# Optimization experiments

Measured on AMD Instinct MI355X. Metric: run time of the kernel, lower is better.

## Reference

```python
import jax, jax.numpy as jnp
import numpy as np

H = 1024  # hidden size

def _gru_layer(x, h0_l, w_ih_l, w_hh_l, b_ih_l, b_hh_l):
    # x: [T,B,I]; precompute input gates for all timesteps (like addmm in the kernel)
    x_gates = jnp.einsum('tbi,gi->tbg', x, w_ih_l) + b_ih_l  # [T,B,3H]

    def step(h, xg):
        # h: [B,H]; xg: [B,3H]
        h_gates = h @ w_hh_l.T + b_hh_l  # [B,3H]
        xr, xz, xn = xg[:, :H], xg[:, H:2*H], xg[:, 2*H:]
        hr, hz, hn = h_gates[:, :H], h_gates[:, H:2*H], h_gates[:, 2*H:]
        r = jax.nn.sigmoid(xr + hr)
        z = jax.nn.sigmoid(xz + hz)
        n = jnp.tanh(xn + r * hn)
        h_new = (1.0 - z) * n + z * h
        return h_new, h_new

    h_final, seq_out = jax.lax.scan(step, h0_l, x_gates)
    return h_final, seq_out


def setup_inputs() -> dict:
    key = jax.random.key(0)
    ks = jax.random.split(key, 6)
    T, B, I, L = 512, 64, 1024, 2
    s = 1.0 / np.sqrt(H)
    return {
        'x': jax.random.normal(ks[0], (T, B, I), dtype=jnp.float32),
        'h0': jax.random.normal(ks[1], (L, B, H), dtype=jnp.float32),
        'w_ih': jax.random.normal(ks[2], (L, 3 * H, I), dtype=jnp.float32) * s,
        'w_hh': jax.random.normal(ks[3], (L, 3 * H, H), dtype=jnp.float32) * s,
        'b_ih': jax.random.normal(ks[4], (L, 3 * H), dtype=jnp.float32) * s,
        'b_hh': jax.random.normal(ks[5], (L, 3 * H), dtype=jnp.float32) * s,
    }


def reference(x, h0, w_ih, w_hh, b_ih, b_hh):
    num_layers = h0.shape[0]
    h_n = []
    cur = x
    for l in range(num_layers):
        h_final, seq_out = _gru_layer(cur, h0[l], w_ih[l], w_hh[l], b_ih[l], b_hh[l])
        h_n.append(h_final)
        cur = seq_out  # layer output becomes next layer's input
    # kernel returns only the final hidden state of every layer, in fp32
    return jnp.stack(h_n, axis=0)  # [L,B,H]
```

## Files before the change

### kernel.cpp

```cpp
#include <hip/hip_runtime.h>

typedef unsigned short u16;
typedef unsigned long long u64;
typedef __attribute__((ext_vector_type(8))) short short8;
typedef __attribute__((ext_vector_type(4))) float f32x4;

#define HH 1024
#define BB 64
#define TT 512
#define G3 3072
#define NBLK 192
#define NS 513
#define SLOT (BB * HH)
#define FSTRIDE 32

__device__ __forceinline__ u16 f2b(float f) {
  unsigned u = __float_as_uint(f);
  unsigned r = (u + 0x7fffu + ((u >> 16) & 1u)) >> 16;
  return (u16)r;
}
__device__ __forceinline__ float b2f(u16 h) {
  return __uint_as_float(((unsigned)h) << 16);
}

__device__ __forceinline__ void st_u32_agent(unsigned* p, unsigned v) {
  __hip_atomic_store(p, v, __ATOMIC_RELAXED, __HIP_MEMORY_SCOPE_AGENT);
}
__device__ __forceinline__ unsigned ld_u32_agent(const unsigned* p) {
  return __hip_atomic_load(p, __ATOMIC_RELAXED, __HIP_MEMORY_SCOPE_AGENT);
}


__global__ void f32_to_bf16_k(const float* __restrict__ s, u16* __restrict__ d, int n) {
  int stride = gridDim.x * blockDim.x * 4;
  for (int i = (blockIdx.x * blockDim.x + threadIdx.x) * 4; i < n; i += stride) {
    float4 v = *(const float4*)(s + i);
    uint2 p;
    p.x = (unsigned)f2b(v.x) | ((unsigned)f2b(v.y) << 16);
    p.y = (unsigned)f2b(v.z) | ((unsigned)f2b(v.w) << 16);
    *(uint2*)(d + i) = p;
  }
}

__global__ void init_h_k(const float* __restrict__ h0in, u16* __restrict__ hbuf0,
                         u16* __restrict__ hbuf1) {
  int i = blockIdx.x * blockDim.x + threadIdx.x;
  if (i < BB * HH) {
    hbuf0[i] = f2b(h0in[i]);
    hbuf1[i] = f2b(h0in[BB * HH + i]);
  }
}


__global__ __launch_bounds__(256) void gemm_xg_k(
    const u16* __restrict__ A, const u16* __restrict__ Wt,
    const float* __restrict__ bias, u16* __restrict__ C) {
  const int bm = blockIdx.x / 24;
  const int bn = blockIdx.x % 24;
  const int m0 = bm * 128, n0 = bn * 128;
  __shared__ __align__(16) u16 al[128 * 40];
  __shared__ __align__(16) u16 bl[128 * 40];
  const int tid = threadIdx.x;
  const int w = tid >> 6, l = tid & 63;
  const int wr = w >> 1, wc = w & 1;
  const int c0 = tid, c1 = tid + 256;
  const int r0 = c0 >> 2, s0 = c0 & 3, r1 = c1 >> 2, s1 = c1 & 3;

  const f32x4 fzero = {0.f, 0.f, 0.f, 0.f};
  f32x4 acc[4][4];
#pragma unroll
  for (int i = 0; i < 4; ++i)
#pragma unroll
    for (int j = 0; j < 4; ++j) acc[i][j] = fzero;

  const u16* a0p = A + (size_t)(m0 + r0) * 1024 + s0 * 8;
  const u16* a1p = A + (size_t)(m0 + r1) * 1024 + s1 * 8;
  const u16* b0p = Wt + (size_t)(n0 + r0) * 1024 + s0 * 8;
  const u16* b1p = Wt + (size_t)(n0 + r1) * 1024 + s1 * 8;

  int4 va0 = *(const int4*)(a0p);
  int4 va1 = *(const int4*)(a1p);
  int4 vb0 = *(const int4*)(b0p);
  int4 vb1 = *(const int4*)(b1p);

  for (int kt = 0; kt < 32; ++kt) {
    __syncthreads();
    *(int4*)&al[r0 * 40 + s0 * 8] = va0;
    *(int4*)&al[r1 * 40 + s1 * 8] = va1;
    *(int4*)&bl[r0 * 40 + s0 * 8] = vb0;
    *(int4*)&bl[r1 * 40 + s1 * 8] = vb1;
    __syncthreads();
    if (kt < 31) {
      va0 = *(const int4*)(a0p + (kt + 1) * 32);
      va1 = *(const int4*)(a1p + (kt + 1) * 32);
      vb0 = *(const int4*)(b0p + (kt + 1) * 32);
      vb1 = *(const int4*)(b1p + (kt + 1) * 32);
    }
    short8 af[4], bf[4];
#pragma unroll
    for (int i = 0; i < 4; ++i)
      af[i] = *(const short8*)&al[(wr * 64 + i * 16 + (l & 15)) * 40 + (l >> 4) * 8];
#pragma unroll
    for (int j = 0; j < 4; ++j)
      bf[j] = *(const short8*)&bl[(wc * 64 + j * 16 + (l & 15)) * 40 + (l >> 4) * 8];
#pragma unroll
    for (int i = 0; i < 4; ++i)
#pragma unroll
      for (int j = 0; j < 4; ++j)
        acc[i][j] = __builtin_amdgcn_mfma_f32_16x16x32_bf16(af[i], bf[j], acc[i][j], 0, 0, 0);
  }

#pragma unroll
  for (int i = 0; i < 4; ++i) {
#pragma unroll
    for (int j = 0; j < 4; ++j) {
      int col = n0 + wc * 64 + j * 16 + (l & 15);
      float bv = bias[col];
#pragma unroll
      for (int q = 0; q < 4; ++q) {
        int row = m0 + wr * 64 + i * 16 + (l >> 4) * 4 + q;
        C[(size_t)row * G3 + col] = f2b(acc[i][j][q] + bv);
      }
    }
  }
}


__global__ __launch_bounds__(256, 1) void gru_scan8_k(
    const u16* __restrict__ xg0,
    const u16* __restrict__ whh0, const u16* __restrict__ wih1,
    const u16* __restrict__ whh1,
    const float* __restrict__ bhh0, const float* __restrict__ bih1,
    const float* __restrict__ bhh1,
    const float* __restrict__ h0in,
    u16* __restrict__ hbuf0, u16* __restrict__ hbuf1,
    float* __restrict__ out, unsigned* __restrict__ flags) {
  const int blk = blockIdx.x;
  const int part0 = (blk < 64);
  const int tid = threadIdx.x;
  const int w = tid >> 6, l = tid & 63;
  const int lrow = l & 15;
  const int lr7 = lrow & 7;
  const int kb = (l >> 4) * 8;
  const int myrow0 = w * 16 + (l >> 4) * 4;
  const size_t arow = (size_t)(w * 16 + lrow) * HH + kb;
  const f32x4 fzero = {0.f, 0.f, 0.f, 0.f};

  __shared__ __align__(16) u16 wlds[48 * 1024];

  int j;
  float hreg[4] = {0.f, 0.f, 0.f, 0.f};
  float bhr = 0.f, bhz = 0.f, bhn = 0.f;
  float bir = 0.f, biz = 0.f, bin = 0.f;
  bool valid;

  if (part0) {
    const int sub = blk;
    j = sub * 16 + lrow;
    valid = true;
    for (int i = tid; i < 6144; i += 256) {
      int r = i >> 7;
      int c = i & 127;
      int g = r >> 4;
      int wrow = g * HH + sub * 16 + (r & 15);
      int4 v = *(const int4*)(whh0 + (size_t)wrow * 1024 + c * 8);
      int idx = r * 1024 + ((c * 8) ^ ((r & 7) << 3));
      *(int4*)&wlds[idx] = v;
    }
    bhr = bhh0[j]; bhz = bhh0[HH + j]; bhn = bhh0[2 * HH + j];
#pragma unroll
    for (int q = 0; q < 4; ++q) hreg[q] = h0in[(myrow0 + q) * HH + j];
  } else {
    const int sub = blk - 64;
    valid = (lrow < 8);
    j = sub * 8 + (valid ? lrow : 0);
    for (int i = tid; i < 6144; i += 256) {
      int r = i >> 7;
      int c = i & 127;
      int half = r >= 24;
      int rr = half ? r - 24 : r;
      int g = rr >> 3;
      const u16* src = half ? wih1 : whh1;
      int wrow = g * HH + sub * 8 + (rr & 7);
      int4 v = *(const int4*)(src + (size_t)wrow * 1024 + c * 8);
      int idx = r * 1024 + ((c * 8) ^ ((r & 7) << 3));
      *(int4*)&wlds[idx] = v;
    }
    bhr = bhh1[j]; bhz = bhh1[HH + j]; bhn = bhh1[2 * HH + j];
    bir = bih1[j]; biz = bih1[HH + j]; bin = bih1[2 * HH + j];
#pragma unroll
    for (int q = 0; q < 4; ++q) hreg[q] = h0in[BB * HH + (myrow0 + q) * HH + j];
  }
  __syncthreads();

  const int sx = lr7 << 3;

  for (int t = 0; t <= 512; ++t) {
    if (part0) {
      if (t <= 511) {
        const u16* Ap = hbuf0 + (size_t)t * SLOT + arow;
        short8 ar[32];
#pragma unroll
        for (int ks = 0; ks < 32; ++ks) ar[ks] = *(const short8*)(Ap + ks * 32);

        u16 xrv[4], xzv[4], xnv[4];
        const u16* xp = xg0 + (size_t)t * BB * G3;
#pragma unroll
        for (int q = 0; q < 4; ++q) {
          const u16* rp = xp + (size_t)(myrow0 + q) * G3;
          xrv[q] = rp[j]; xzv[q] = rp[HH + j]; xnv[q] = rp[2 * HH + j];
        }

        f32x4 acc0 = fzero, acc1 = fzero, acc2 = fzero;
#pragma unroll
        for (int ks = 0; ks < 32; ++ks) {
          int ke = kb + ks * 32;
          short8 b0 = *(const short8*)&wlds[(lrow) * 1024 + (ke ^ sx)];
          short8 b1 = *(const short8*)&wlds[(16 + lrow) * 1024 + (ke ^ sx)];
          short8 b2 = *(const short8*)&wlds[(32 + lrow) * 1024 + (ke ^ sx)];
          acc0 = __builtin_amdgcn_mfma_f32_16x16x32_bf16(ar[ks], b0, acc0, 0, 0, 0);
          acc1 = __builtin_amdgcn_mfma_f32_16x16x32_bf16(ar[ks], b1, acc1, 0, 0, 0);
          acc2 = __builtin_amdgcn_mfma_f32_16x16x32_bf16(ar[ks], b2, acc2, 0, 0, 0);
        }

        u16* hbn = hbuf0 + (size_t)(t + 1) * SLOT;
#pragma unroll
        for (int q = 0; q < 4; ++q) {
          float rr = acc0[q] + bhr + b2f(xrv[q]);
          float zz = acc1[q] + bhz + b2f(xzv[q]);
          float nn = acc2[q] + bhn;
          float r = 1.f / (1.f + __expf(-rr));
          float z = 1.f / (1.f + __expf(-zz));
          float n = tanhf(b2f(xnv[q]) + r * nn);
          float hv = (1.f - z) * n + z * hreg[q];
          hreg[q] = hv;
          int hb = (int)f2b(hv);
          int nb = __shfl_xor(hb, 1);
          if ((l & 1) == 0) {
            unsigned pk = (unsigned)(u16)hb | (((unsigned)(u16)nb) << 16);
            st_u32_agent((unsigned*)(hbn + (size_t)(myrow0 + q) * HH + j), pk);
          }
        }
      }
    } else {
      if (t >= 1) {
        const u16* Ai = hbuf0 + (size_t)t * SLOT + arow;
        short8 ar[32];
#pragma unroll
        for (int ks = 0; ks < 32; ++ks) ar[ks] = *(const short8*)(Ai + ks * 32);
        f32x4 xri = fzero, xzi = fzero, xni = fzero;
#pragma unroll
        for (int ks = 0; ks < 32; ++ks) {
          int ke = kb + ks * 32;
          short8 b0 = *(const short8*)&wlds[(24 + lr7) * 1024 + (ke ^ sx)];
          short8 b1 = *(const short8*)&wlds[(32 + lr7) * 1024 + (ke ^ sx)];
          short8 b2 = *(const short8*)&wlds[(40 + lr7) * 1024 + (ke ^ sx)];
          xri = __builtin_amdgcn_mfma_f32_16x16x32_bf16(ar[ks], b0, xri, 0, 0, 0);
          xzi = __builtin_amdgcn_mfma_f32_16x16x32_bf16(ar[ks], b1, xzi, 0, 0, 0);
          xni = __builtin_amdgcn_mfma_f32_16x16x32_bf16(ar[ks], b2, xni, 0, 0, 0);
        }
        const u16* Ah = hbuf1 + (size_t)(t - 1) * SLOT + arow;
#pragma unroll
        for (int ks = 0; ks < 32; ++ks) ar[ks] = *(const short8*)(Ah + ks * 32);
        f32x4 hri = fzero, hzi = fzero, hni = fzero;
#pragma unroll
        for (int ks = 0; ks < 32; ++ks) {
          int ke = kb + ks * 32;
          short8 b0 = *(const short8*)&wlds[(0 + lr7) * 1024 + (ke ^ sx)];
          short8 b1 = *(const short8*)&wlds[(8 + lr7) * 1024 + (ke ^ sx)];
          short8 b2 = *(const short8*)&wlds[(16 + lr7) * 1024 + (ke ^ sx)];
          hri = __builtin_amdgcn_mfma_f32_16x16x32_bf16(ar[ks], b0, hri, 0, 0, 0);
          hzi = __builtin_amdgcn_mfma_f32_16x16x32_bf16(ar[ks], b1, hzi, 0, 0, 0);
          hni = __builtin_amdgcn_mfma_f32_16x16x32_bf16(ar[ks], b2, hni, 0, 0, 0);
        }

        u16* hbn = hbuf1 + (size_t)t * SLOT;
#pragma unroll
        for (int q = 0; q < 4; ++q) {
          float rr = (xri[q] + bir) + (hri[q] + bhr);
          float zz = (xzi[q] + biz) + (hzi[q] + bhz);
          float nn = hni[q] + bhn;
          float r = 1.f / (1.f + __expf(-rr));
          float z = 1.f / (1.f + __expf(-zz));
          float n = tanhf((xni[q] + bin) + r * nn);
          float hv = (1.f - z) * n + z * hreg[q];
          hreg[q] = hv;
          int hb = (int)f2b(hv);
          int nb = __shfl_xor(hb, 1);
          if (valid && (l & 1) == 0) {
            unsigned pk = (unsigned)(u16)hb | (((unsigned)(u16)nb) << 16);
            st_u32_agent((unsigned*)(hbn + (size_t)(myrow0 + q) * HH + j), pk);
          }
        }
      }
    }

    __syncthreads();
    if (tid == 0) {
      __builtin_amdgcn_fence(__ATOMIC_RELEASE, "workgroup");
      st_u32_agent(&flags[blk * FSTRIDE], (unsigned)(t + 1));
    }
    if (tid < 64) {
      const unsigned tgt = (unsigned)(t + 1);
      for (;;) {
        unsigned a0 = ld_u32_agent(&flags[l * FSTRIDE]);
        unsigned a1 = ld_u32_agent(&flags[(l + 64) * FSTRIDE]);
        unsigned a2 = ld_u32_agent(&flags[(l + 128) * FSTRIDE]);
        unsigned mn = a0 < a1 ? a0 : a1;
        mn = mn < a2 ? mn : a2;
        if (__all(mn >= tgt)) break;
        __builtin_amdgcn_s_sleep(2);
      }
    }
    __syncthreads();
    __builtin_amdgcn_fence(__ATOMIC_ACQUIRE, "workgroup");
  }

  if (part0) {
#pragma unroll
    for (int q = 0; q < 4; ++q) out[(size_t)(myrow0 + q) * HH + j] = hreg[q];
  } else if (valid) {
#pragma unroll
    for (int q = 0; q < 4; ++q) out[BB * HH + (size_t)(myrow0 + q) * HH + j] = hreg[q];
  }
}


extern "C" void kernel_launch(void* const* d_in, const int* in_sizes, int n_in,
                              void* d_out, int out_size, void* d_ws, size_t ws_size,
                              hipStream_t stream) {
  const float* x   = (const float*)d_in[0];
  const float* h0  = (const float*)d_in[1];
  const float* wih = (const float*)d_in[2];
  const float* whh = (const float*)d_in[3];
  const float* bih = (const float*)d_in[4];
  const float* bhh = (const float*)d_in[5];
  float* out = (float*)d_out;

  char* ws = (char*)d_ws;
  size_t off = 0;
  auto alloc = [&](size_t bytes) -> void* {
    void* p = ws + off;
    off += (bytes + 255) & ~(size_t)255;
    return p;
  };
  u16* xg0   = (u16*)alloc((size_t)TT * BB * G3 * 2);
  u16* wihb  = (u16*)alloc((size_t)2 * G3 * HH * 2);
  u16* whhb  = (u16*)alloc((size_t)2 * G3 * HH * 2);
  size_t hbytes = (size_t)2 * NS * SLOT * 2;
  size_t xbytes = (size_t)TT * BB * HH * 2;
  char* un = (char*)alloc(hbytes > xbytes ? hbytes : xbytes);
  u16* xbf   = (u16*)un;
  u16* hbuf0 = (u16*)un;
  u16* hbuf1 = hbuf0 + (size_t)NS * SLOT;
  unsigned* flags = (unsigned*)alloc(NBLK * FSTRIDE * 4);

  hipMemsetAsync(flags, 0, NBLK * FSTRIDE * 4, stream);
  f32_to_bf16_k<<<2048, 256, 0, stream>>>(x, xbf, TT * BB * HH);
  f32_to_bf16_k<<<512, 256, 0, stream>>>(wih, wihb, 2 * G3 * HH);
  f32_to_bf16_k<<<512, 256, 0, stream>>>(whh, whhb, 2 * G3 * HH);

  gemm_xg_k<<<6144, 256, 0, stream>>>(xbf, wihb, bih, xg0);

  init_h_k<<<256, 256, 0, stream>>>(h0, hbuf0, hbuf1);

  gru_scan8_k<<<NBLK, 256, 0, stream>>>(xg0,
                                        whhb, wihb + (size_t)G3 * HH, whhb + (size_t)G3 * HH,
                                        bhh, bih + G3, bhh + G3, h0,
                                        hbuf0, hbuf1, out, flags);
}
```

Measured before the change: 5.467 ms.

## Replace global per-step barrier with per-layer dependency flags in GRU scan

The single all-blocks barrier per timestep is split into separate loops for the two layers, each with its own wait condition. Layer-0 blocks wait only on the other layer-0 blocks' flags for step t. Layer-1 blocks wait on layer-0 reaching step t and on layer-1 reaching step t-1, so layer 0 can run ahead and the two layers no longer run in lockstep. Layer-1 also loads both A operands before its two MFMA loops, and the spin sleep is shortened. This removes cross-layer stalls and barrier overhead. It relies on every timestep having its own hbuf slot so that running ahead cannot overwrite data still being read, and it uses more registers for the two operand arrays.

```diff
diff --git a/kernel.cpp b/kernel.cpp
--- a/kernel.cpp
+++ b/kernel.cpp
@@ -126,7 +126,7 @@
 }
 
 
-__global__ __launch_bounds__(256, 1) void gru_scan8_k(
+__global__ __launch_bounds__(256, 1) void gru_scan9_k(
     const u16* __restrict__ xg0,
     const u16* __restrict__ whh0, const u16* __restrict__ wih1,
     const u16* __restrict__ whh1,
@@ -148,16 +148,9 @@
 
   __shared__ __align__(16) u16 wlds[48 * 1024];
 
-  int j;
-  float hreg[4] = {0.f, 0.f, 0.f, 0.f};
-  float bhr = 0.f, bhz = 0.f, bhn = 0.f;
-  float bir = 0.f, biz = 0.f, bin = 0.f;
-  bool valid;
-
   if (part0) {
     const int sub = blk;
-    j = sub * 16 + lrow;
-    valid = true;
+    const int j = sub * 16 + lrow;
     for (int i = tid; i < 6144; i += 256) {
       int r = i >> 7;
       int c = i & 127;
@@ -167,13 +160,83 @@
       int idx = r * 1024 + ((c * 8) ^ ((r & 7) << 3));
       *(int4*)&wlds[idx] = v;
     }
-    bhr = bhh0[j]; bhz = bhh0[HH + j]; bhn = bhh0[2 * HH + j];
+    const float bhr = bhh0[j], bhz = bhh0[HH + j], bhn = bhh0[2 * HH + j];
+    float hreg[4];
 #pragma unroll
     for (int q = 0; q < 4; ++q) hreg[q] = h0in[(myrow0 + q) * HH + j];
+    __syncthreads();
+    const int sx = lr7 << 3;
+
+    for (int t = 0; t < TT; ++t) {
+      if (t > 0) {
+        if (tid < 64) {
+          for (;;) {
+            unsigned a0 = ld_u32_agent(&flags[l * FSTRIDE]);
+            if (__all(a0 >= (unsigned)t)) break;
+            __builtin_amdgcn_s_sleep(1);
+          }
+        }
+        __syncthreads();
+        __builtin_amdgcn_fence(__ATOMIC_ACQUIRE, "workgroup");
+      }
+
+      const u16* Ap = hbuf0 + (size_t)t * SLOT + arow;
+      short8 ar[32];
+#pragma unroll
+      for (int ks = 0; ks < 32; ++ks) ar[ks] = *(const short8*)(Ap + ks * 32);
+
+      u16 xrv[4], xzv[4], xnv[4];
+      const u16* xp = xg0 + (size_t)t * BB * G3;
+#pragma unroll
+      for (int q = 0; q < 4; ++q) {
+        const u16* rp = xp + (size_t)(myrow0 + q) * G3;
+        xrv[q] = rp[j]; xzv[q] = rp[HH + j]; xnv[q] = rp[2 * HH + j];
+      }
+
+      f32x4 acc0 = fzero, acc1 = fzero, acc2 = fzero;
+#pragma unroll
+      for (int ks = 0; ks < 32; ++ks) {
+        int ke = kb + ks * 32;
+        short8 b0 = *(const short8*)&wlds[(lrow) * 1024 + (ke ^ sx)];
+        short8 b1 = *(const short8*)&wlds[(16 + lrow) * 1024 + (ke ^ sx)];
+        short8 b2 = *(const short8*)&wlds[(32 + lrow) * 1024 + (ke ^ sx)];
+        acc0 = __builtin_amdgcn_mfma_f32_16x16x32_bf16(ar[ks], b0, acc0, 0, 0, 0);
+        acc1 = __builtin_amdgcn_mfma_f32_16x16x32_bf16(ar[ks], b1, acc1, 0, 0, 0);
+        acc2 = __builtin_amdgcn_mfma_f32_16x16x32_bf16(ar[ks], b2, acc2, 0, 0, 0);
+      }
+
+      u16* hbn = hbuf0 + (size_t)(t + 1) * SLOT;
+#pragma unroll
+      for (int q = 0; q < 4; ++q) {
+        float rr = acc0[q] + bhr + b2f(xrv[q]);
+        float zz = acc1[q] + bhz + b2f(xzv[q]);
+        float nn = acc2[q] + bhn;
+        float r = 1.f / (1.f + __expf(-rr));
+        float z = 1.f / (1.f + __expf(-zz));
+        float n = tanhf(b2f(xnv[q]) + r * nn);
+        float hv = (1.f - z) * n + z * hreg[q];
+        hreg[q] = hv;
+        int hb = (int)f2b(hv);
+        int nb = __shfl_xor(hb, 1);
+        if ((l & 1) == 0) {
+          unsigned pk = (unsigned)(u16)hb | (((unsigned)(u16)nb) << 16);
+          st_u32_agent((unsigned*)(hbn + (size_t)(myrow0 + q) * HH + j), pk);
+        }
+      }
+
+      __syncthreads();
+      if (tid == 0) {
+        __builtin_amdgcn_fence(__ATOMIC_RELEASE, "workgroup");
+        st_u32_agent(&flags[blk * FSTRIDE], (unsigned)(t + 1));
+      }
+    }
+#pragma unroll
+    for (int q = 0; q < 4; ++q) out[(size_t)(myrow0 + q) * HH + j] = hreg[q];
+
   } else {
     const int sub = blk - 64;
-    valid = (lrow < 8);
-    j = sub * 8 + (valid ? lrow : 0);
+    const bool valid = (lrow < 8);
+    const int j = sub * 8 + (valid ? lrow : 0);
     for (int i = tid; i < 6144; i += 256) {
       int r = i >> 7;
       int c = i & 127;
@@ -186,142 +249,89 @@
       int idx = r * 1024 + ((c * 8) ^ ((r & 7) << 3));
       *(int4*)&wlds[idx] = v;
     }
-    bhr = bhh1[j]; bhz = bhh1[HH + j]; bhn = bhh1[2 * HH + j];
-    bir = bih1[j]; biz = bih1[HH + j]; bin = bih1[2 * HH + j];
+    const float bhr = bhh1[j], bhz = bhh1[HH + j], bhn = bhh1[2 * HH + j];
+    const float bir = bih1[j], biz = bih1[HH + j], bin = bih1[2 * HH + j];
+    float hreg[4];
 #pragma unroll
     for (int q = 0; q < 4; ++q) hreg[q] = h0in[BB * HH + (myrow0 + q) * HH + j];
-  }
-  __syncthreads();
-
-  const int sx = lr7 << 3;
-
-  for (int t = 0; t <= 512; ++t) {
-    if (part0) {
-      if (t <= 511) {
-        const u16* Ap = hbuf0 + (size_t)t * SLOT + arow;
-        short8 ar[32];
-#pragma unroll
-        for (int ks = 0; ks < 32; ++ks) ar[ks] = *(const short8*)(Ap + ks * 32);
-
-        u16 xrv[4], xzv[4], xnv[4];
-        const u16* xp = xg0 + (size_t)t * BB * G3;
-#pragma unroll
-        for (int q = 0; q < 4; ++q) {
-          const u16* rp = xp + (size_t)(myrow0 + q) * G3;
-          xrv[q] = rp[j]; xzv[q] = rp[HH + j]; xnv[q] = rp[2 * HH + j];
+    __syncthreads();
+    const int sx = lr7 << 3;
+
+    for (int t = 1; t <= TT; ++t) {
+      if (tid < 64) {
+        for (;;) {
+          unsigned a0 = ld_u32_agent(&flags[l * FSTRIDE]);
+          unsigned a1 = ld_u32_agent(&flags[(64 + l) * FSTRIDE]);
+          unsigned a2 = ld_u32_agent(&flags[(128 + l) * FSTRIDE]);
+          unsigned mn = a1 < a2 ? a1 : a2;
+          int ok = (a0 >= (unsigned)t) && (mn >= (unsigned)(t - 1));
+          if (__all(ok)) break;
+          __builtin_amdgcn_s_sleep(1);
         }
-
-        f32x4 acc0 = fzero, acc1 = fzero, acc2 = fzero;
-#pragma unroll
-        for (int ks = 0; ks < 32; ++ks) {
-          int ke = kb + ks * 32;
-          short8 b0 = *(const short8*)&wlds[(lrow) * 1024 + (ke ^ sx)];
-          short8 b1 = *(const short8*)&wlds[(16 + lrow) * 1024 + (ke ^ sx)];
-          short8 b2 = *(const short8*)&wlds[(32 + lrow) * 1024 + (ke ^ sx)];
-          acc0 = __builtin_amdgcn_mfma_f32_16x16x32_bf16(ar[ks], b0, acc0, 0, 0, 0);
-          acc1 = __builtin_amdgcn_mfma_f32_16x16x32_bf16(ar[ks], b1, acc1, 0, 0, 0);
-          acc2 = __builtin_amdgcn_mfma_f32_16x16x32_bf16(ar[ks], b2, acc2, 0, 0, 0);
+      }
+      __syncthreads();
+      __builtin_amdgcn_fence(__ATOMIC_ACQUIRE, "workgroup");
+
+      const u16* Ai = hbuf0 + (size_t)t * SLOT + arow;
+      const u16* Ah = hbuf1 + (size_t)(t - 1) * SLOT + arow;
+      short8 ai[32], ah[32];
+#pragma unroll
+      for (int ks = 0; ks < 32; ++ks) ai[ks] = *(const short8*)(Ai + ks * 32);
+#pragma unroll
+      for (int ks = 0; ks < 32; ++ks) ah[ks] = *(const short8*)(Ah + ks * 32);
+
+      f32x4 xri = fzero, xzi = fzero, xni = fzero;
+#pragma unroll
+      for (int ks = 0; ks < 32; ++ks) {
+        int ke = kb + ks * 32;
+        short8 b0 = *(const short8*)&wlds[(24 + lr7) * 1024 + (ke ^ sx)];
+        short8 b1 = *(const short8*)&wlds[(32 + lr7) * 1024 + (ke ^ sx)];
+        short8 b2 = *(const short8*)&wlds[(40 + lr7) * 1024 + (ke ^ sx)];
+        xri = __builtin_amdgcn_mfma_f32_16x16x32_bf16(ai[ks], b0, xri, 0, 0, 0);
+        xzi = __builtin_amdgcn_mfma_f32_16x16x32_bf16(ai[ks], b1, xzi, 0, 0, 0);
+        xni = __builtin_amdgcn_mfma_f32_16x16x32_bf16(ai[ks], b2, xni, 0, 0, 0);
+      }
+      f32x4 hri = fzero, hzi = fzero, hni = fzero;
+#pragma unroll
+      for (int ks = 0; ks < 32; ++ks) {
+        int ke = kb + ks * 32;
+        short8 b0 = *(const short8*)&wlds[(0 + lr7) * 1024 + (ke ^ sx)];
+        short8 b1 = *(const short8*)&wlds[(8 + lr7) * 1024 + (ke ^ sx)];
+        short8 b2 = *(const short8*)&wlds[(16 + lr7) * 1024 + (ke ^ sx)];
+        hri = __builtin_amdgcn_mfma_f32_16x16x32_bf16(ah[ks], b0, hri, 0, 0, 0);
+        hzi = __builtin_amdgcn_mfma_f32_16x16x32_bf16(ah[ks], b1, hzi, 0, 0, 0);
+        hni = __builtin_amdgcn_mfma_f32_16x16x32_bf16(ah[ks], b2, hni, 0, 0, 0);
+      }
+
+      u16* hbn = hbuf1 + (size_t)t * SLOT;
+#pragma unroll
+      for (int q = 0; q < 4; ++q) {
+        float rr = (xri[q] + bir) + (hri[q] + bhr);
+        float zz = (xzi[q] + biz) + (hzi[q] + bhz);
+        float nn = hni[q] + bhn;
+        float r = 1.f / (1.f + __expf(-rr));
+        float z = 1.f / (1.f + __expf(-zz));
+        float n = tanhf((xni[q] + bin) + r * nn);
+        float hv = (1.f - z) * n + z * hreg[q];
+        hreg[q] = hv;
+        int hb = (int)f2b(hv);
+        int nb = __shfl_xor(hb, 1);
+        if (valid && (l & 1) == 0) {
+          unsigned pk = (unsigned)(u16)hb | (((unsigned)(u16)nb) << 16);
+          st_u32_agent((unsigned*)(hbn + (size_t)(myrow0 + q) * HH + j), pk);
         }
-
-        u16* hbn = hbuf0 + (size_t)(t + 1) * SLOT;
-#pragma unroll
-        for (int q = 0; q < 4; ++q) {
-          float rr = acc0[q] + bhr + b2f(xrv[q]);
-          float zz = acc1[q] + bhz + b2f(xzv[q]);
-          float nn = acc2[q] + bhn;
-          float r = 1.f / (1.f + __expf(-rr));
-          float z = 1.f / (1.f + __expf(-zz));
-          float n = tanhf(b2f(xnv[q]) + r * nn);
-          float hv = (1.f - z) * n + z * hreg[q];
-          hreg[q] = hv;
-          int hb = (int)f2b(hv);
-          int nb = __shfl_xor(hb, 1);
-          if ((l & 1) == 0) {
-            unsigned pk = (unsigned)(u16)hb | (((unsigned)(u16)nb) << 16);
-            st_u32_agent((unsigned*)(hbn + (size_t)(myrow0 + q) * HH + j), pk);
-          }
-        }
-      }
-    } else {
-      if (t >= 1) {
-        const u16* Ai = hbuf0 + (size_t)t * SLOT + arow;
-        short8 ar[32];
-#pragma unroll
-        for (int ks = 0; ks < 32; ++ks) ar[ks] = *(const short8*)(Ai + ks * 32);
-        f32x4 xri = fzero, xzi = fzero, xni = fzero;
-#pragma unroll
-        for (int ks = 0; ks < 32; ++ks) {
-          int ke = kb + ks * 32;
-          short8 b0 = *(const short8*)&wlds[(24 + lr7) * 1024 + (ke ^ sx)];
-          short8 b1 = *(const short8*)&wlds[(32 + lr7) * 1024 + (ke ^ sx)];
-          short8 b2 = *(const short8*)&wlds[(40 + lr7) * 1024 + (ke ^ sx)];
-          xri = __builtin_amdgcn_mfma_f32_16x16x32_bf16(ar[ks], b0, xri, 0, 0, 0);
-          xzi = __builtin_amdgcn_mfma_f32_16x16x32_bf16(ar[ks], b1, xzi, 0, 0, 0);
-          xni = __builtin_amdgcn_mfma_f32_16x16x32_bf16(ar[ks], b2, xni, 0, 0, 0);
-        }
-        const u16* Ah = hbuf1 + (size_t)(t - 1) * SLOT + arow;
-#pragma unroll
-        for (int ks = 0; ks < 32; ++ks) ar[ks] = *(const short8*)(Ah + ks * 32);
-        f32x4 hri = fzero, hzi = fzero, hni = fzero;
-#pragma unroll
-        for (int ks = 0; ks < 32; ++ks) {
-          int ke = kb + ks * 32;
-          short8 b0 = *(const short8*)&wlds[(0 + lr7) * 1024 + (ke ^ sx)];
-          short8 b1 = *(const short8*)&wlds[(8 + lr7) * 1024 + (ke ^ sx)];
-          short8 b2 = *(const short8*)&wlds[(16 + lr7) * 1024 + (ke ^ sx)];
-          hri = __builtin_amdgcn_mfma_f32_16x16x32_bf16(ar[ks], b0, hri, 0, 0, 0);
-          hzi = __builtin_amdgcn_mfma_f32_16x16x32_bf16(ar[ks], b1, hzi, 0, 0, 0);
-          hni = __builtin_amdgcn_mfma_f32_16x16x32_bf16(ar[ks], b2, hni, 0, 0, 0);
-        }
-
-        u16* hbn = hbuf1 + (size_t)t * SLOT;
-#pragma unroll
-        for (int q = 0; q < 4; ++q) {
-          float rr = (xri[q] + bir) + (hri[q] + bhr);
-          float zz = (xzi[q] + biz) + (hzi[q] + bhz);
-          float nn = hni[q] + bhn;
-          float r = 1.f / (1.f + __expf(-rr));
-          float z = 1.f / (1.f + __expf(-zz));
-          float n = tanhf((xni[q] + bin) + r * nn);
-          float hv = (1.f - z) * n + z * hreg[q];
-          hreg[q] = hv;
-          int hb = (int)f2b(hv);
-          int nb = __shfl_xor(hb, 1);
-          if (valid && (l & 1) == 0) {
-            unsigned pk = (unsigned)(u16)hb | (((unsigned)(u16)nb) << 16);
-            st_u32_agent((unsigned*)(hbn + (size_t)(myrow0 + q) * HH + j), pk);
-          }
-        }
-      }
-    }
-
-    __syncthreads();
-    if (tid == 0) {
-      __builtin_amdgcn_fence(__ATOMIC_RELEASE, "workgroup");
-      st_u32_agent(&flags[blk * FSTRIDE], (unsigned)(t + 1));
-    }
-    if (tid < 64) {
-      const unsigned tgt = (unsigned)(t + 1);
-      for (;;) {
-        unsigned a0 = ld_u32_agent(&flags[l * FSTRIDE]);
-        unsigned a1 = ld_u32_agent(&flags[(l + 64) * FSTRIDE]);
-        unsigned a2 = ld_u32_agent(&flags[(l + 128) * FSTRIDE]);
-        unsigned mn = a0 < a1 ? a0 : a1;
-        mn = mn < a2 ? mn : a2;
-        if (__all(mn >= tgt)) break;
-        __builtin_amdgcn_s_sleep(2);
-      }
-    }
-    __syncthreads();
-    __builtin_amdgcn_fence(__ATOMIC_ACQUIRE, "workgroup");
-  }
-
-  if (part0) {
-#pragma unroll
-    for (int q = 0; q < 4; ++q) out[(size_t)(myrow0 + q) * HH + j] = hreg[q];
-  } else if (valid) {
-#pragma unroll
-    for (int q = 0; q < 4; ++q) out[BB * HH + (size_t)(myrow0 + q) * HH + j] = hreg[q];
+      }
+
+      __syncthreads();
+      if (tid == 0) {
+        __builtin_amdgcn_fence(__ATOMIC_RELEASE, "workgroup");
+        st_u32_agent(&flags[blk * FSTRIDE], (unsigned)t);
+      }
+    }
+    if (valid) {
+#pragma unroll
+      for (int q = 0; q < 4; ++q) out[BB * HH + (size_t)(myrow0 + q) * HH + j] = hreg[q];
+    }
   }
 }
 
@@ -364,7 +374,7 @@
 
   init_h_k<<<256, 256, 0, stream>>>(h0, hbuf0, hbuf1);
 
-  gru_scan8_k<<<NBLK, 256, 0, stream>>>(xg0,
+  gru_scan9_k<<<NBLK, 256, 0, stream>>>(xg0,
                                         whhb, wihb + (size_t)G3 * HH, whhb + (size_t)G3 * HH,
                                         bhh, bih + G3, bhh + G3, h0,
                                         hbuf0, hbuf1, out, flags);
```

New measurement: 5.542 ms. No clear change (+1.4%).
